# Kernel optimization log

Hardware: AMD Instinct MI355X
Metric: run time of the kernel (lower is better)

The kernel has to match this reference:

```python
import jax, jax.numpy as jnp
import numpy as np

H = 16
D_MODEL = 1024
D_K = D_MODEL // H


def setup_inputs() -> dict:
    key = jax.random.key(0)
    ks = jax.random.split(key, 11)
    B, S = 2, 2048
    scale = 1.0 / np.sqrt(D_MODEL)
    inp = {
        "query": jax.random.normal(ks[0], (B, S, D_MODEL), dtype=jnp.float32),
        "key": jax.random.normal(ks[1], (B, S, D_MODEL), dtype=jnp.float32),
        "value": jax.random.normal(ks[2], (B, S, D_MODEL), dtype=jnp.float32),
        "Wq": jax.random.normal(ks[3], (D_MODEL, D_MODEL), dtype=jnp.float32) * scale,
        "bq": jnp.zeros((D_MODEL,), dtype=jnp.float32),
        "Wk": jax.random.normal(ks[4], (D_MODEL, D_MODEL), dtype=jnp.float32) * scale,
        "bk": jnp.zeros((D_MODEL,), dtype=jnp.float32),
        "Wv": jax.random.normal(ks[5], (D_MODEL, D_MODEL), dtype=jnp.float32) * scale,
        "bv": jnp.zeros((D_MODEL,), dtype=jnp.float32),
        "Wo": jax.random.normal(ks[6], (D_MODEL, D_MODEL), dtype=jnp.float32) * scale,
        "bo": jnp.zeros((D_MODEL,), dtype=jnp.float32),
    }
    return inp


def _mha(query, key, value, Wq, bq, Wk, bk, Wv, bv, Wo, bo):
    B, S, _ = query.shape
    # linear projections (torch nn.Linear: x @ W.T + b)
    q = query @ Wq.T + bq
    k = key @ Wk.T + bk
    v = value @ Wv.T + bv
    # split heads: [B, S, D] -> [B, H, S, d_k]
    q = q.reshape(B, S, H, D_K).transpose(0, 2, 1, 3)
    k = k.reshape(B, S, H, D_K).transpose(0, 2, 1, 3)
    v = v.reshape(B, S, H, D_K).transpose(0, 2, 1, 3)
    # scaled dot-product attention with manual stable softmax
    scores = jnp.einsum("bhqd,bhkd->bhqk", q, k) / jnp.sqrt(jnp.float32(D_K))
    stable = scores - jnp.max(scores, axis=-1, keepdims=True)
    e = jnp.exp(stable)
    attn = e / jnp.sum(e, axis=-1, keepdims=True)
    ctx = jnp.einsum("bhqk,bhkd->bhqd", attn, v)
    # merge heads and final projection
    ctx = ctx.transpose(0, 2, 1, 3).reshape(B, S, H * D_K)
    return ctx @ Wo.T + bo


def reference(query, key, value, Wq, bq, Wk, bk, Wv, bv, Wo, bo):
    return _mha(query, key, value, Wq, bq, Wk, bk, Wv, bv, Wo, bo)
```

## Files before the change

kernel.cpp:

```cpp
#include <hip/hip_runtime.h>


#define S_LEN 2048
#define BATCH 2
#define DM    1024
#define NH    16
#define DKH   64
#define BS    (BATCH * S_LEN)

typedef _Float16 f16x8 __attribute__((ext_vector_type(8)));
typedef _Float16 f16x4 __attribute__((ext_vector_type(4)));
typedef _Float16 f16x2 __attribute__((ext_vector_type(2)));
typedef __fp16   h16x2 __attribute__((ext_vector_type(2)));
typedef float    f32x4 __attribute__((ext_vector_type(4)));
typedef float    f32x16 __attribute__((ext_vector_type(16)));

__device__ __forceinline__ f16x2 pk_f16(float a, float b) {
  h16x2 r = __builtin_amdgcn_cvt_pkrtz(a, b);
  return __builtin_bit_cast(f16x2, r);
}

__device__ __forceinline__ void gld16(const void* g, void* l) {
  __builtin_amdgcn_global_load_lds(
      (const __attribute__((address_space(1))) void*)g,
      (__attribute__((address_space(3))) void*)l, 16, 0, 0);
}

__device__ __forceinline__ float fast_exp2(float x) {
#if __has_builtin(__builtin_amdgcn_exp2f)
  return __builtin_amdgcn_exp2f(x);
#else
  return exp2f(x);
#endif
}

__device__ __forceinline__ int swap23(int x) {
  return (x & ~12) | ((x & 4) << 1) | ((x & 8) >> 1);
}

__global__ __launch_bounds__(256) void cvt_all(
    const float* __restrict__ q, const float* __restrict__ k, const float* __restrict__ v,
    const float* __restrict__ wq, const float* __restrict__ wk,
    const float* __restrict__ wv, const float* __restrict__ wo,
    _Float16* __restrict__ xq, _Float16* __restrict__ xk, _Float16* __restrict__ xv,
    _Float16* __restrict__ w16)
{
  const int y = blockIdx.y;
  const float* src; _Float16* dst; int n;
  if (y == 0)      { src = q;  dst = xq; n = BS * DM; }
  else if (y == 1) { src = k;  dst = xk; n = BS * DM; }
  else if (y == 2) { src = v;  dst = xv; n = BS * DM; }
  else {
    src = (y == 3) ? wq : ((y == 4) ? wk : ((y == 5) ? wv : wo));
    dst = w16 + (size_t)(y - 3) * (DM * DM);
    n = DM * DM;
  }
  int i0 = (blockIdx.x * 256 + threadIdx.x) * 4;
  if (i0 < n) {
    float4 f = *(const float4*)(src + i0);
    f16x2 lo = pk_f16(f.x, f.y);
    f16x2 hi = pk_f16(f.z, f.w);
    f16x4 hh; hh[0] = lo[0]; hh[1] = lo[1]; hh[2] = hi[0]; hh[3] = hi[1];
    *(f16x4*)(dst + i0) = hh;
  }
}

template <typename OUT_T, bool VT>
__device__ __forceinline__ void gemm_core(
    const _Float16* __restrict__ A, const _Float16* __restrict__ W,
    const float* __restrict__ bias, OUT_T* __restrict__ out, float oscale)
{
  const int tid  = threadIdx.x;
  const int l    = tid & 63;
  const int wv   = tid >> 6;
  const int c    = l & 15, quad = l >> 4;
  const int m0   = blockIdx.y * 128, n0 = blockIdx.x * 128;
  const int wm   = wv & 1, wn = wv >> 1;
  __shared__ _Float16 sA[128 * 64];
  __shared__ _Float16 sB[128 * 64];

  const _Float16* gA[4]; const _Float16* gB[4];
#pragma unroll
  for (int p = 0; p < 4; ++p) {
    int s = tid + p * 256, r = s >> 3, g = (s & 7) ^ (r & 7);
    gA[p] = A + (size_t)(m0 + r) * DM + g * 8;
    gB[p] = W + (size_t)(n0 + r) * DM + g * 8;
  }
  const int cx = c & 7;

  f32x4 acc[4][4] = {};
  for (int k0 = 0; k0 < DM; k0 += 64) {
    __syncthreads();
#pragma unroll
    for (int p = 0; p < 4; ++p) {
      gld16(gA[p] + k0, sA + (tid + p * 256) * 8);
      gld16(gB[p] + k0, sB + (tid + p * 256) * 8);
    }
    __syncthreads();
#pragma unroll
    for (int ks = 0; ks < 2; ++ks) {
      f16x8 af[4], bf[4];
#pragma unroll
      for (int i = 0; i < 4; ++i)
        af[i] = *(const f16x8*)&sA[(wm * 64 + i * 16 + c) * 64 + ((ks * 4 + quad) ^ cx) * 8];
#pragma unroll
      for (int j = 0; j < 4; ++j)
        bf[j] = *(const f16x8*)&sB[(wn * 64 + j * 16 + c) * 64 + ((ks * 4 + quad) ^ cx) * 8];
#pragma unroll
      for (int i = 0; i < 4; ++i)
#pragma unroll
        for (int j = 0; j < 4; ++j)
          acc[i][j] = __builtin_amdgcn_mfma_f32_16x16x32_f16(af[i], bf[j], acc[i][j], 0, 0, 0);
    }
  }
  if constexpr (VT) {
#pragma unroll
    for (int j = 0; j < 4; ++j) {
      int col = n0 + wn * 64 + j * 16 + c;
      float bb = bias[col];
      int hh = col >> 6, dd = col & 63;
#pragma unroll
      for (int i = 0; i < 4; ++i) {
        int row = m0 + wm * 64 + i * 16 + quad * 4;
        int bb2 = row >> 11, ss = row & (S_LEN - 1);
        _Float16* dst = (_Float16*)out + ((size_t)(bb2 * NH + hh) * DKH + dd) * S_LEN + ss;
        f16x4 v4;
#pragma unroll
        for (int r = 0; r < 4; ++r) v4[r] = (_Float16)((acc[i][j][r] + bb) * oscale);
        *(f16x4*)dst = v4;
      }
    }
  } else {
#pragma unroll
    for (int j = 0; j < 4; ++j) {
      int col = n0 + wn * 64 + j * 16 + c;
      float bb = bias[col];
#pragma unroll
      for (int i = 0; i < 4; ++i) {
        int row = m0 + wm * 64 + i * 16 + quad * 4;
#pragma unroll
        for (int r = 0; r < 4; ++r) {
          float vv = (acc[i][j][r] + bb) * oscale;
          out[(size_t)(row + r) * DM + col] = (OUT_T)vv;
        }
      }
    }
  }
}

#define SC_Q (0.125f * 1.44269504088896340736f)

__global__ __launch_bounds__(256) void proj3(
    const _Float16* __restrict__ xq, const _Float16* __restrict__ xk,
    const _Float16* __restrict__ xv, const _Float16* __restrict__ w16,
    const float* __restrict__ bq, const float* __restrict__ bk, const float* __restrict__ bv,
    _Float16* __restrict__ Q, _Float16* __restrict__ K, _Float16* __restrict__ Vt)
{
  const int z = blockIdx.z;
  if (z == 2) {
    gemm_core<_Float16, true>(xv, w16 + (size_t)2 * DM * DM, bv, Vt, 1.0f);
  } else if (z == 0) {
    gemm_core<_Float16, false>(xq, w16, bq, Q, SC_Q);
  } else {
    gemm_core<_Float16, false>(xk, w16 + (size_t)DM * DM, bk, K, 1.0f);
  }
}

__global__ __launch_bounds__(256) void out_gemm(
    const _Float16* __restrict__ ctx, const _Float16* __restrict__ wo,
    const float* __restrict__ bo, float* __restrict__ out)
{
  gemm_core<float, false>(ctx, wo, bo, out, 1.0f);
}

__global__ __launch_bounds__(256, 2) void attn(
    const _Float16* __restrict__ Q, const _Float16* __restrict__ K,
    const _Float16* __restrict__ Vt, _Float16* __restrict__ ctx)
{
  const int tid = threadIdx.x;
  const int l   = tid & 63, wv = tid >> 6;
  const int lo5 = l & 31, hf = l >> 5;
  const int q0  = blockIdx.x * 128;
  const int bh  = blockIdx.y;
  const int b   = bh >> 4, hd = bh & 15;
  __shared__ _Float16 sK[2][64 * 64];
  __shared__ _Float16 sV[2][64 * 64];

  f16x8 qf[4];
  {
    const _Float16* Qg = Q + ((size_t)(b * S_LEN + q0 + wv * 32 + lo5)) * DM + hd * DKH + 8 * hf;
#pragma unroll
    for (int kc = 0; kc < 4; ++kc) qf[kc] = *(const f16x8*)(Qg + 16 * kc);
  }

  f32x16 o[2] = {};
  float l_part = 0.f;
  const f16x2 ones = {(_Float16)1.0f, (_Float16)1.0f};

  const _Float16* Kg0 = K + ((size_t)b * S_LEN) * DM + hd * DKH;
  const _Float16* Vg0 = Vt + ((size_t)bh * DKH) * S_LEN;

  const int sa = tid,       ra = sa >> 3, ba = (sa & 7) ^ (ra & 7);
  const int sb = tid + 256, rb = sb >> 3, bb = (sb & 7) ^ (rb & 7);
  const _Float16* gKa = Kg0 + (size_t)swap23(ra) * DM + ba * 8;
  const _Float16* gKb = Kg0 + (size_t)swap23(rb) * DM + bb * 8;
  const _Float16* gVa = Vg0 + (size_t)ra * S_LEN + ba * 8;
  const _Float16* gVb = Vg0 + (size_t)rb * S_LEN + bb * 8;
  const int rx = lo5 & 7;

  gld16(gKa, sK[0] + sa * 8);
  gld16(gKb, sK[0] + sb * 8);
  gld16(gVa, sV[0] + sa * 8);
  gld16(gVb, sV[0] + sb * 8);
  __syncthreads();

  for (int kt = 0; kt < S_LEN / 64; ++kt) {
    const int cur = kt & 1;
    const int nk = (kt < S_LEN / 64 - 1) ? (kt + 1) : kt;
    const size_t k0n = (size_t)nk * 64;
    gld16(gKa + k0n * DM, sK[cur ^ 1] + sa * 8);
    gld16(gKb + k0n * DM, sK[cur ^ 1] + sb * 8);
    gld16(gVa + k0n,      sV[cur ^ 1] + sa * 8);
    gld16(gVb + k0n,      sV[cur ^ 1] + sb * 8);

    f32x16 sAcc[2] = {};
#pragma unroll
    for (int kb = 0; kb < 2; ++kb)
#pragma unroll
      for (int kc = 0; kc < 4; ++kc) {
        f16x8 kf = *(const f16x8*)&sK[cur][(32 * kb + lo5) * 64 + ((2 * kc + hf) ^ rx) * 8];
        sAcc[kb] = __builtin_amdgcn_mfma_f32_32x32x16_f16(kf, qf[kc], sAcc[kb], 0, 0, 0);
      }

    f16x8 pPv[2][2];
#pragma unroll
    for (int kb = 0; kb < 2; ++kb)
#pragma unroll
      for (int half = 0; half < 2; ++half)
#pragma unroll
        for (int j2 = 0; j2 < 4; ++j2) {
          float p0 = fast_exp2(sAcc[kb][8 * half + 2 * j2]);
          float p1 = fast_exp2(sAcc[kb][8 * half + 2 * j2 + 1]);
          f16x2 pk = pk_f16(p0, p1);
          pPv[kb][half][2 * j2]     = pk[0];
          pPv[kb][half][2 * j2 + 1] = pk[1];
          l_part = __builtin_amdgcn_fdot2(__builtin_bit_cast(h16x2, pk),
                                          __builtin_bit_cast(h16x2, ones), l_part, false);
        }

#pragma unroll
    for (int db = 0; db < 2; ++db)
#pragma unroll
      for (int kc2 = 0; kc2 < 4; ++kc2) {
        f16x8 vf = *(const f16x8*)&sV[cur][(32 * db + lo5) * 64 + ((2 * kc2 + hf) ^ rx) * 8];
        o[db] = __builtin_amdgcn_mfma_f32_32x32x16_f16(pPv[kc2 >> 1][kc2 & 1], vf, o[db], 0, 0, 0);
      }

    __syncthreads();
  }

  l_part += __shfl_xor(l_part, 32);
  float* lsum = (float*)&sK[0][0] + wv * 32;
  if (hf == 0) lsum[lo5] = l_part;
  float inv[16];
#pragma unroll
  for (int r = 0; r < 16; ++r) {
    int qq = 8 * (r >> 2) + 4 * hf + (r & 3);
    inv[r] = 1.0f / lsum[qq];
  }

  _Float16* Og = ctx + ((size_t)(b * S_LEN + q0 + wv * 32)) * DM + hd * DKH;
#pragma unroll
  for (int db = 0; db < 2; ++db)
#pragma unroll
    for (int r = 0; r < 16; ++r) {
      int qq = 8 * (r >> 2) + 4 * hf + (r & 3);
      Og[(size_t)qq * DM + 32 * db + lo5] = (_Float16)(o[db][r] * inv[r]);
    }
}

extern "C" void kernel_launch(void* const* d_in, const int* in_sizes, int n_in,
                              void* d_out, int out_size, void* d_ws, size_t ws_size,
                              hipStream_t stream)
{
  (void)in_sizes; (void)n_in; (void)out_size; (void)ws_size;
  const float* q  = (const float*)d_in[0];
  const float* k  = (const float*)d_in[1];
  const float* v  = (const float*)d_in[2];
  const float* wq = (const float*)d_in[3];
  const float* bq = (const float*)d_in[4];
  const float* wk = (const float*)d_in[5];
  const float* bk = (const float*)d_in[6];
  const float* wv = (const float*)d_in[7];
  const float* bv = (const float*)d_in[8];
  const float* wo = (const float*)d_in[9];
  const float* bo = (const float*)d_in[10];

  char* ws = (char*)d_ws;
  _Float16* XQ  = (_Float16*)(ws);
  _Float16* XK  = (_Float16*)(ws + (8u  << 20));
  _Float16* XV  = (_Float16*)(ws + (16u << 20));
  _Float16* W16 = (_Float16*)(ws + (24u << 20));
  _Float16* Qp  = (_Float16*)(ws + (32u << 20));
  _Float16* Kp  = (_Float16*)(ws + (40u << 20));
  _Float16* VT  = (_Float16*)(ws + (48u << 20));
  _Float16* CTX = XQ;
  float* out = (float*)d_out;

  cvt_all<<<dim3(4096, 7), 256, 0, stream>>>(q, k, v, wq, wk, wv, wo, XQ, XK, XV, W16);
  proj3<<<dim3(8, 32, 3), 256, 0, stream>>>(XQ, XK, XV, W16, bq, bk, bv, Qp, Kp, VT);
  attn<<<dim3(16, 32), 256, 0, stream>>>(Qp, Kp, VT, CTX);
  out_gemm<<<dim3(8, 32), 256, 0, stream>>>(CTX, W16 + (size_t)3 * DM * DM, bo, out);
}
```

Baseline: 231.6 us.

## Triple-buffer K/V tiles in attention with vmcnt waits and MFMA priority

Converts the attention loop's double-buffered K/V LDS staging into a three-deep ring, prefetching two tiles ahead. The end-of-iteration __syncthreads is replaced by a partial s_waitcnt vmcnt plus a raw barrier at the top of each iteration, so one tile's loads stay in flight during compute. s_setprio raises wave priority around the MFMA sections. The cost is 50% more LDS per block, and correctness now depends on hand-written waitcnt counts.

```diff
diff --git a/kernel.cpp b/kernel.cpp
--- a/kernel.cpp
+++ b/kernel.cpp
@@ -183,8 +183,8 @@
   const int q0  = blockIdx.x * 128;
   const int bh  = blockIdx.y;
   const int b   = bh >> 4, hd = bh & 15;
-  __shared__ _Float16 sK[2][64 * 64];
-  __shared__ _Float16 sV[2][64 * 64];
+  __shared__ _Float16 sK[3][64 * 64];
+  __shared__ _Float16 sV[3][64 * 64];
 
   f16x8 qf[4];
   {
@@ -208,29 +208,42 @@
   const _Float16* gVb = Vg0 + (size_t)rb * S_LEN + bb * 8;
   const int rx = lo5 & 7;
 
-  gld16(gKa, sK[0] + sa * 8);
-  gld16(gKb, sK[0] + sb * 8);
-  gld16(gVa, sV[0] + sa * 8);
-  gld16(gVb, sV[0] + sb * 8);
-  __syncthreads();
-
+#define STAGE(t, bf) do {                                   \
+    const size_t k0s = (size_t)(t) * 64;                    \
+    gld16(gKa + k0s * DM, sK[bf] + sa * 8);                 \
+    gld16(gKb + k0s * DM, sK[bf] + sb * 8);                 \
+    gld16(gVa + k0s,      sV[bf] + sa * 8);                 \
+    gld16(gVb + k0s,      sV[bf] + sb * 8);                 \
+  } while (0)
+
+  STAGE(0, 0);
+  STAGE(1, 1);
+
+  int cur = 0;
   for (int kt = 0; kt < S_LEN / 64; ++kt) {
-    const int cur = kt & 1;
-    const int nk = (kt < S_LEN / 64 - 1) ? (kt + 1) : kt;
-    const size_t k0n = (size_t)nk * 64;
-    gld16(gKa + k0n * DM, sK[cur ^ 1] + sa * 8);
-    gld16(gKb + k0n * DM, sK[cur ^ 1] + sb * 8);
-    gld16(gVa + k0n,      sV[cur ^ 1] + sa * 8);
-    gld16(gVb + k0n,      sV[cur ^ 1] + sb * 8);
+    if (kt == S_LEN / 64 - 1)
+      asm volatile("s_waitcnt vmcnt(0)" ::: "memory");
+    else
+      asm volatile("s_waitcnt vmcnt(4)" ::: "memory");
+    __builtin_amdgcn_s_barrier();
+    if (kt < S_LEN / 64 - 2) {
+      int nb = cur + 2; if (nb >= 3) nb -= 3;
+      STAGE(kt + 2, nb);
+    }
+
+    const _Float16* sKc = sK[cur];
+    const _Float16* sVc = sV[cur];
 
     f32x16 sAcc[2] = {};
+    __builtin_amdgcn_s_setprio(1);
 #pragma unroll
     for (int kb = 0; kb < 2; ++kb)
 #pragma unroll
       for (int kc = 0; kc < 4; ++kc) {
-        f16x8 kf = *(const f16x8*)&sK[cur][(32 * kb + lo5) * 64 + ((2 * kc + hf) ^ rx) * 8];
+        f16x8 kf = *(const f16x8*)&sKc[(32 * kb + lo5) * 64 + ((2 * kc + hf) ^ rx) * 8];
         sAcc[kb] = __builtin_amdgcn_mfma_f32_32x32x16_f16(kf, qf[kc], sAcc[kb], 0, 0, 0);
       }
+    __builtin_amdgcn_s_setprio(0);
 
     f16x8 pPv[2][2];
 #pragma unroll
@@ -248,16 +261,19 @@
                                           __builtin_bit_cast(h16x2, ones), l_part, false);
         }
 
+    __builtin_amdgcn_s_setprio(1);
 #pragma unroll
     for (int db = 0; db < 2; ++db)
 #pragma unroll
       for (int kc2 = 0; kc2 < 4; ++kc2) {
-        f16x8 vf = *(const f16x8*)&sV[cur][(32 * db + lo5) * 64 + ((2 * kc2 + hf) ^ rx) * 8];
+        f16x8 vf = *(const f16x8*)&sVc[(32 * db + lo5) * 64 + ((2 * kc2 + hf) ^ rx) * 8];
         o[db] = __builtin_amdgcn_mfma_f32_32x32x16_f16(pPv[kc2 >> 1][kc2 & 1], vf, o[db], 0, 0, 0);
       }
-
-    __syncthreads();
-  }
+    __builtin_amdgcn_s_setprio(0);
+
+    cur = (cur == 2) ? 0 : cur + 1;
+  }
+#undef STAGE
 
   l_part += __shfl_xor(l_part, 32);
   float* lsum = (float*)&sK[0][0] + wv * 32;
```

Result: no change. 229.7 us (-0.8%).
